# Kernel tuning notes

Measured on AMD Instinct MI355X. Metric: run time of the kernel, lower is better.

Reference implementation:

```python
import jax, jax.numpy as jnp
import numpy as np

T, K, H, I, E = 8192, 2, 1024, 2816, 8


def setup_inputs() -> dict:
    key = jax.random.key(0)
    k1, k2, k3, k4, k5 = jax.random.split(key, 5)
    hidden_states = jax.random.normal(k1, (T, H), dtype=jnp.float32)
    expert_routing_table = jax.random.randint(k2, (T, K), 0, E)
    router_weights = jax.random.uniform(k3, (T, K), dtype=jnp.float32)
    # permuted_weights=True: weights stored so forward is x @ w
    # w13: fused gate+up proj [E, H, 2I]; w2: down proj [E, I, H]
    w13 = jax.random.normal(k4, (E, H, 2 * I), dtype=jnp.float32) * (1.0 / np.sqrt(H))
    w2 = jax.random.normal(k5, (E, I, H), dtype=jnp.float32) * (1.0 / np.sqrt(I))
    return {
        "hidden_states": hidden_states,
        "expert_routing_table": expert_routing_table,
        "router_weights": router_weights,
        "w13": w13,
        "w2": w2,
    }


def reference(hidden_states, expert_routing_table, router_weights, w13, w2):
    # Semantics of hpu.mixture_of_experts with activation='silu':
    # out[t] = sum_k rw[t,k] * ( (silu(x@w1g[e]) * (x@w1u[e])) @ w2[e] ), e = table[t,k]
    n_experts = w13.shape[0]
    inter = w2.shape[1]
    # per-token combine coefficient for each expert: [T, E]
    onehot = jax.nn.one_hot(expert_routing_table, n_experts, dtype=hidden_states.dtype)  # [T,K,E]
    coeff = jnp.einsum("tke,tk->te", onehot, router_weights)
    out = jnp.zeros_like(hidden_states)
    for e in range(n_experts):
        gu = hidden_states @ w13[e]            # [T, 2I]
        gate, up = gu[:, :inter], gu[:, inter:]
        h = jax.nn.silu(gate) * up             # [T, I]
        out = out + coeff[:, e:e + 1] * (h @ w2[e])
    return out
```

## Files before the change

### kernel.cpp

```cpp
#include <hip/hip_runtime.h>

typedef unsigned short u16;
typedef unsigned int u32;
typedef __bf16 bf16x8 __attribute__((ext_vector_type(8)));
typedef float f32x4 __attribute__((ext_vector_type(4)));
typedef u16 u16x8 __attribute__((ext_vector_type(8)));

#define T_TOK 8192
#define HDIM 1024
#define IDIM 2816
#define NEXP 8
#define NPAIR (T_TOK * 2)
#define MAXRB 71

#define XB_OFF   (147456u)
#define W13T_OFF (XB_OFF + 16777216u)
#define W2T_OFF  (W13T_OFF + 92274688u)
#define H_OFF    (W2T_OFF + 46137344u)
#define WS_NEED  ((size_t)H_OFF + 102367232u)

__device__ __forceinline__ u16 f2bf(float f) {
  u32 u = __builtin_bit_cast(u32, f);
  u32 r = u + 0x7fffu + ((u >> 16) & 1u);
  return (u16)(r >> 16);
}

#define GLD16(g, l) __builtin_amdgcn_global_load_lds( \
    (const __attribute__((address_space(1))) void*)(g), \
    (__attribute__((address_space(3))) void*)(l), 16, 0, 0)

#define WAITVM(N) asm volatile("s_waitcnt vmcnt(" #N ")" ::: "memory")

__device__ __forceinline__ void sbar() {
  asm volatile("" ::: "memory");
  __builtin_amdgcn_s_barrier();
  asm volatile("" ::: "memory");
}

__device__ __forceinline__ void pbar() {
  __builtin_amdgcn_sched_barrier(0);
  asm volatile("" ::: "memory");
  __builtin_amdgcn_s_barrier();
  asm volatile("" ::: "memory");
  __builtin_amdgcn_sched_barrier(0);
}

__global__ void fillinit_k(int* __restrict__ pairs, int* __restrict__ meta) {
  if (blockIdx.x == 0 && threadIdx.x < 16) meta[threadIdx.x] = 0;
  pairs[blockIdx.x * 256 + threadIdx.x] = -1;
}

__global__ void count_k(const int* __restrict__ routing, int* __restrict__ meta) {
  int i = blockIdx.x * 256 + threadIdx.x;
  if (i < NPAIR) atomicAdd(&meta[routing[i]], 1);
}

__global__ void scan_k(int* __restrict__ meta) {
  if (threadIdx.x == 0) {
    int rb = 0;
    for (int e = 0; e < NEXP; ++e) {
      meta[16 + e] = rb * 256;
      int nrb = (meta[e] + 255) >> 8;
      for (int i = 0; i < nrb; ++i) meta[32 + rb + i] = e;
      rb += nrb;
    }
    meta[24] = rb;
  }
}

__global__ void scatter_k(const int* __restrict__ routing, int* __restrict__ meta,
                          int* __restrict__ pairs, int* __restrict__ inv) {
  int i = blockIdx.x * 256 + threadIdx.x;
  if (i < NPAIR) {
    int e = routing[i];
    int pos = atomicAdd(&meta[8 + e], 1);
    int row = meta[16 + e] + pos;
    pairs[row] = i;
    inv[i] = row;
  }
}

__global__ void conv_x(const float* __restrict__ in, u16* __restrict__ out) {
  int i = blockIdx.x * 256 + threadIdx.x;
  float4 a = ((const float4*)in)[2 * i];
  float4 b = ((const float4*)in)[2 * i + 1];
  u16x8 o = { f2bf(a.x), f2bf(a.y), f2bf(a.z), f2bf(a.w),
              f2bf(b.x), f2bf(b.y), f2bf(b.z), f2bf(b.w) };
  ((u16x8*)out)[i] = o;
}

#define TSW(r, c) (((((c) >> 2) ^ ((((r) >> 4) & 3) << 2)) << 2) | ((c) & 3))
__global__ void transpose_cvt(const float* __restrict__ in, u16* __restrict__ out,
                              int R, int C) {
  __shared__ float tile[64][68];
  size_t base = (size_t)blockIdx.z * (size_t)R * (size_t)C;
  in += base; out += base;
  int t = threadIdx.x;
  int r0 = blockIdx.y * 64, c0 = blockIdx.x * 64;
  int lr = t >> 4, cb = t & 15;
#pragma unroll
  for (int p = 0; p < 4; ++p) {
    int row = p * 16 + lr;
    float4 v = *(const float4*)&in[(size_t)(r0 + row) * C + c0 + cb * 4];
    int pc = ((cb ^ ((p & 3) << 2)) << 2);
    tile[row][pc] = v.x; tile[row][pc + 1] = v.y;
    tile[row][pc + 2] = v.z; tile[row][pc + 3] = v.w;
  }
  __syncthreads();
  int oc = t >> 2, g0 = (t & 3) * 2;
#pragma unroll
  for (int gg = 0; gg < 2; ++gg) {
    int g = g0 + gg;
    u16x8 o = { f2bf(tile[g * 8 + 0][TSW(g * 8 + 0, oc)]), f2bf(tile[g * 8 + 1][TSW(g * 8 + 1, oc)]),
                f2bf(tile[g * 8 + 2][TSW(g * 8 + 2, oc)]), f2bf(tile[g * 8 + 3][TSW(g * 8 + 3, oc)]),
                f2bf(tile[g * 8 + 4][TSW(g * 8 + 4, oc)]), f2bf(tile[g * 8 + 5][TSW(g * 8 + 5, oc)]),
                f2bf(tile[g * 8 + 6][TSW(g * 8 + 6, oc)]), f2bf(tile[g * 8 + 7][TSW(g * 8 + 7, oc)]) };
    *(u16x8*)&out[(size_t)(c0 + oc) * R + r0 + g * 8] = o;
  }
}

__global__ __launch_bounds__(512, 2) void gemm1_k(
    const u16* __restrict__ Xb, const u16* __restrict__ W13T,
    const int* __restrict__ pairs, const int* __restrict__ meta,
    const float* __restrict__ rwf, u16* __restrict__ Hb) {
  int lin = blockIdx.x + 22 * blockIdx.y;
  int xcd = lin & 7, slot = lin >> 3;
  int flat = (xcd < 2) ? xcd * 196 + slot : 392 + (xcd - 2) * 195 + slot;
  int bx = flat / 71, rb = flat % 71;
  if (rb >= meta[24]) return;
  const int e = meta[32 + rb];
  const int bn0 = bx * 128;
  const int tid = threadIdx.x, lane = tid & 63, w = tid >> 6;
  const int wr = w >> 2, wc = w & 3;
  const int rowBase = rb * 256;

  __shared__ __align__(16) u16 lds[65536];
  char* const lb = (char*)lds;

  const int tr = tid >> 3;
  const int swk = ((tid & 7) << 4) ^ ((tr & 7) << 4);
  const u16* aS[4]; const u16* bS[4];
  const u16* wBase = W13T + (size_t)e * (2 * IDIM) * HDIM;
#pragma unroll
  for (int s = 0; s < 4; ++s) {
    int pr = pairs[rowBase + s * 64 + tr];
    int tok = pr < 0 ? 0 : (pr >> 1);
    aS[s] = Xb + (size_t)tok * HDIM + (swk >> 1);
    bS[s] = wBase + (size_t)((tr >> 5) * IDIM + bn0 + s * 32 + (tr & 31)) * HDIM + (swk >> 1);
  }

#define STGA(b, h, kt) { GLD16(aS[(h)*2]   + (kt)*64, lb + (b)*32768 + (h)*16384 + tid*16); \
                         GLD16(aS[(h)*2+1] + (kt)*64, lb + (b)*32768 + (h)*16384 + 8192 + tid*16); }
#define STGB(b, h, kt) { GLD16(bS[(h)*2]   + (kt)*64, lb + 65536 + (b)*32768 + (h)*16384 + tid*16); \
                         GLD16(bS[(h)*2+1] + (kt)*64, lb + 65536 + (b)*32768 + (h)*16384 + 8192 + tid*16); }

  const int l15 = lane & 15, l4 = lane >> 4, l7 = lane & 7;
  const int ko0 = (l4 * 16) ^ (l7 << 4);
  const int ko1 = (64 + l4 * 16) ^ (l7 << 4);
  const int aFB = wr * 16384 + l15 * 128;
  const int bFB = 65536 + (wc * 64 + l15) * 128;

#define LDA(d, b, mh, mf, ko) d = *(const bf16x8*)(lb + (b)*32768 + aFB + (mh)*8192 + (mf)*2048 + (ko))
#define LDB(d, b, nf, ko)     d = *(const bf16x8*)(lb + (b)*32768 + bFB + (nf)*2048 + (ko))

#define MFQ(mh, A, B) \
  _Pragma("unroll") for (int mf = 0; mf < 4; ++mf) \
  _Pragma("unroll") for (int nf = 0; nf < 4; ++nf) \
    acc[(mh)*4+mf][nf] = __builtin_amdgcn_mfma_f32_16x16x32_bf16(A[mf], B[nf], acc[(mh)*4+mf][nf], 0, 0, 0);

  f32x4 acc[8][4];
  const f32x4 fz = {0.f, 0.f, 0.f, 0.f};
#pragma unroll
  for (int i = 0; i < 8; ++i)
#pragma unroll
    for (int j = 0; j < 4; ++j) acc[i][j] = fz;

  STGB(0, 0, 0); STGB(0, 1, 0); STGA(0, 0, 0); STGA(0, 1, 0); STGB(1, 0, 1); STGB(1, 1, 1);
  WAITVM(4);
  sbar();

  bf16x8 aA[4], aB[4], bK0[4], bK1[4];
#pragma unroll
  for (int f = 0; f < 4; ++f) { LDA(aA[f], 0, 0, f, ko0); LDB(bK0[f], 0, f, ko0); }

#define TILE1(b, t1, t2) { \
     \
    _Pragma("unroll") for (int f = 0; f < 4; ++f) { LDA(aB[f], b, 0, f, ko1); LDB(bK1[f], b, f, ko1); } \
    STGA((b)^1, 0, t1); \
    sbar(); \
    __builtin_amdgcn_s_setprio(1); MFQ(0, aA, bK0); __builtin_amdgcn_s_setprio(0); \
    sbar(); \
     \
    _Pragma("unroll") for (int f = 0; f < 4; ++f) { LDA(aA[f], b, 1, f, ko0); } \
    STGA((b)^1, 1, t1); \
    sbar(); \
    __builtin_amdgcn_s_setprio(1); MFQ(0, aB, bK1); __builtin_amdgcn_s_setprio(0); \
    sbar(); \
     \
    _Pragma("unroll") for (int f = 0; f < 4; ++f) { LDA(aB[f], b, 1, f, ko1); } \
    STGB(b, 0, t2); \
    sbar(); \
    __builtin_amdgcn_s_setprio(1); MFQ(1, aA, bK0); __builtin_amdgcn_s_setprio(0); \
    sbar(); \
     \
    WAITVM(2); \
    _Pragma("unroll") for (int f = 0; f < 4; ++f) { LDA(aA[f], (b)^1, 0, f, ko0); LDB(bK0[f], (b)^1, f, ko0); } \
    STGB(b, 1, t2); \
    sbar(); \
    __builtin_amdgcn_s_setprio(1); MFQ(1, aB, bK1); __builtin_amdgcn_s_setprio(0); \
    sbar(); \
  }

  for (int jj = 0; jj < 8; ++jj) {
    const int ta = (2 * jj + 1) & 15, tb = (2 * jj + 2) & 15, tc = (2 * jj + 3) & 15;
    TILE1(0, ta, tb);
    TILE1(1, tb, tc);
  }
#undef TILE1
#undef STGA
#undef STGB
#undef LDA
#undef LDB
#undef MFQ

  const int ct = l4;
#pragma unroll
  for (int mf = 0; mf < 8; ++mf) {
#pragma unroll
    for (int j = 0; j < 4; ++j) {
      int m = wr * 128 + mf * 16 + ct * 4 + j;
      int pr = rowBase + m;
      int pair = pairs[pr];
      float rw = pair >= 0 ? rwf[pair] : 0.f;
      u16* hrow = Hb + (size_t)pr * IDIM + bn0 + wc * 32 + l15;
#pragma unroll
      for (int g = 0; g < 2; ++g) {
        float gv = acc[mf][g][j], uv = acc[mf][g + 2][j];
        float s = gv / (1.f + __expf(-gv));
        hrow[g * 16] = f2bf(s * uv * rw);
      }
    }
  }
}

__global__ __launch_bounds__(256, 2) void gemm2_k(
    const u16* __restrict__ Hb, const u16* __restrict__ W2T,
    const int* __restrict__ meta, float* __restrict__ part) {
  int lin = blockIdx.y + 142 * blockIdx.x;
  int xcd = lin & 7, slot = lin >> 3;
  int flat = xcd * 142 + slot;
  int bx = flat / 142, rb2 = flat % 142;
  if (rb2 >= meta[24] * 2) return;
  const int e = meta[32 + (rb2 >> 1)];
  const int bn0 = bx * 128;
  const int tid = threadIdx.x, lane = tid & 63, w = tid >> 6;
  const int wr = w >> 1, wc = w & 1;
  const int rowBase = rb2 * 128;

  __shared__ __align__(16) u16 lds2[32768];
  char* const lb = (char*)lds2;

  const int sr = tid >> 3;
  const int swk = ((tid & 7) << 4) ^ ((sr & 7) << 4);
  const u16* aS[4]; const u16* bS[4];
#pragma unroll
  for (int j = 0; j < 4; ++j) {
    aS[j] = Hb + (size_t)(rowBase + j * 32 + sr) * IDIM + (swk >> 1);
    bS[j] = W2T + (size_t)e * HDIM * IDIM + (size_t)(bn0 + j * 32 + sr) * IDIM + (swk >> 1);
  }

#define STG_A2(b, kt) { GLD16(aS[0] + (kt)*64, lb + (b)*16384 + tid*16); \
                        GLD16(aS[1] + (kt)*64, lb + (b)*16384 + 4096 + tid*16); \
                        GLD16(aS[2] + (kt)*64, lb + (b)*16384 + 8192 + tid*16); \
                        GLD16(aS[3] + (kt)*64, lb + (b)*16384 + 12288 + tid*16); }
#define STG_B2(b, kt) { GLD16(bS[0] + (kt)*64, lb + 32768 + (b)*16384 + tid*16); \
                        GLD16(bS[1] + (kt)*64, lb + 32768 + (b)*16384 + 4096 + tid*16); \
                        GLD16(bS[2] + (kt)*64, lb + 32768 + (b)*16384 + 8192 + tid*16); \
                        GLD16(bS[3] + (kt)*64, lb + 32768 + (b)*16384 + 12288 + tid*16); }

  const int l15 = lane & 15, l4 = lane >> 4, l7 = lane & 7;
  const int ko0 = (l4 * 16) ^ (l7 << 4);
  const int ko1 = (64 + l4 * 16) ^ (l7 << 4);
  const int aFB = (wr * 64 + l15) * 128;
  const int bFB = (wc * 64 + l15) * 128;

#define LDAF2(d, b, mf, ko) d = *(const bf16x8*)(lb + (b)*16384 + aFB + (mf)*2048 + (ko))
#define LDBF2(d, b, nf, ko) d = *(const bf16x8*)(lb + 32768 + (b)*16384 + bFB + (nf)*2048 + (ko))

#define MF16v(A, B) \
  _Pragma("unroll") for (int mf = 0; mf < 4; ++mf) \
  _Pragma("unroll") for (int nf = 0; nf < 4; ++nf) \
    acc[mf][nf] = __builtin_amdgcn_mfma_f32_16x16x32_bf16(A[mf], B[nf], acc[mf][nf], 0, 0, 0);

  f32x4 acc[4][4];
  const f32x4 fz = {0.f, 0.f, 0.f, 0.f};
#pragma unroll
  for (int i = 0; i < 4; ++i)
#pragma unroll
    for (int j = 0; j < 4; ++j) acc[i][j] = fz;

  STG_A2(0, 0); STG_B2(0, 0); STG_A2(1, 1);
  WAITVM(4);
  pbar();

  bf16x8 a0[4], a1[4], b0[4], b1[4];
  for (int i = 0; i < 22; ++i) {
    const int t1 = 2 * i + 1;
    const int nt0 = (2 * i + 2 < 44) ? 2 * i + 2 : 0;
    const int nt1 = (2 * i + 3 < 44) ? 2 * i + 3 : 0;
#pragma unroll
    for (int f = 0; f < 4; ++f) { LDAF2(a0[f], 0, f, ko0); LDAF2(a1[f], 0, f, ko1);
                                  LDBF2(b0[f], 0, f, ko0); LDBF2(b1[f], 0, f, ko1); }
    STG_B2(1, t1);
    pbar();
    __builtin_amdgcn_s_setprio(1); MF16v(a0, b0); __builtin_amdgcn_s_setprio(0);
    pbar();
    STG_A2(0, nt0);
    pbar();
    __builtin_amdgcn_s_setprio(1); MF16v(a1, b1); __builtin_amdgcn_s_setprio(0);
    WAITVM(4);
    pbar();
#pragma unroll
    for (int f = 0; f < 4; ++f) { LDAF2(a0[f], 1, f, ko0); LDAF2(a1[f], 1, f, ko1);
                                  LDBF2(b0[f], 1, f, ko0); LDBF2(b1[f], 1, f, ko1); }
    STG_B2(0, nt0);
    pbar();
    __builtin_amdgcn_s_setprio(1); MF16v(a0, b0); __builtin_amdgcn_s_setprio(0);
    pbar();
    STG_A2(1, nt1);
    pbar();
    __builtin_amdgcn_s_setprio(1); MF16v(a1, b1); __builtin_amdgcn_s_setprio(0);
    WAITVM(4);
    pbar();
  }
#undef STG_A2
#undef STG_B2
#undef LDAF2
#undef LDBF2
#undef MF16v

  WAITVM(0);
  const int ct = l4;
#pragma unroll
  for (int mf = 0; mf < 4; ++mf) {
#pragma unroll
    for (int j = 0; j < 4; ++j) {
      int m = rowBase + wr * 64 + mf * 16 + ct * 4 + j;
      float* prow = part + (size_t)m * HDIM + bn0 + wc * 64 + l15;
#pragma unroll
      for (int nf = 0; nf < 4; ++nf) prow[nf * 16] = acc[mf][nf][j];
    }
  }
}

__global__ void reduce_k(const float* __restrict__ part, const int* __restrict__ inv,
                         float* __restrict__ out) {
  int t = blockIdx.x;
  int c = threadIdx.x * 4;
  int r0 = inv[2 * t], r1 = inv[2 * t + 1];
  float4 a = *(const float4*)&part[(size_t)r0 * HDIM + c];
  float4 b = *(const float4*)&part[(size_t)r1 * HDIM + c];
  float4 o = { a.x + b.x, a.y + b.y, a.z + b.z, a.w + b.w };
  *(float4*)&out[(size_t)t * HDIM + c] = o;
}

extern "C" void kernel_launch(void* const* d_in, const int* in_sizes, int n_in,
                              void* d_out, int out_size, void* d_ws, size_t ws_size,
                              hipStream_t stream) {
  const float* X = (const float*)d_in[0];
  const int* routing = (const int*)d_in[1];
  const float* rwf = (const float*)d_in[2];
  const float* w13 = (const float*)d_in[3];
  const float* w2 = (const float*)d_in[4];
  float* out = (float*)d_out;
  char* ws = (char*)d_ws;

  if (ws_size < WS_NEED) {
    hipMemsetAsync(d_out, 0, (size_t)T_TOK * HDIM * sizeof(float), stream);
    return;
  }

  int* meta = (int*)ws;
  int* pairs = (int*)(ws + 1024);
  int* inv = (int*)(ws + 73728);
  u16* Xb = (u16*)(ws + XB_OFF);
  u16* W13T = (u16*)(ws + W13T_OFF);
  u16* W2T = (u16*)(ws + W2T_OFF);
  u16* Hb = (u16*)(ws + H_OFF);
  float* part = (float*)(ws + W13T_OFF);

  fillinit_k<<<MAXRB, 256, 0, stream>>>(pairs, meta);
  count_k<<<NPAIR / 256, 256, 0, stream>>>(routing, meta);
  scan_k<<<1, 64, 0, stream>>>(meta);
  scatter_k<<<NPAIR / 256, 256, 0, stream>>>(routing, meta, pairs, inv);
  conv_x<<<(T_TOK * HDIM / 8) / 256, 256, 0, stream>>>(X, Xb);
  transpose_cvt<<<dim3(5632 / 64, 1024 / 64, NEXP), 256, 0, stream>>>(w13, W13T, 1024, 5632);
  transpose_cvt<<<dim3(1024 / 64, 2816 / 64, NEXP), 256, 0, stream>>>(w2, W2T, 2816, 1024);
  gemm1_k<<<dim3(22, MAXRB), 512, 0, stream>>>(Xb, W13T, pairs, meta, rwf, Hb);
  gemm2_k<<<dim3(8, 2 * MAXRB), 256, 0, stream>>>(Hb, W2T, meta, part);
  reduce_k<<<T_TOK, 256, 0, stream>>>(part, inv, out);
}
```

Before: 575.9 us.

## Restructure down-projection GEMM to 256x256 tiles with split-K and bf16 partials

The down-projection GEMM now runs 512-thread blocks with 256x256 output tiles, reusing the gemm1 pipelined schedule. The K dimension is split in two (1408 each) to keep the grid size up, and partial results are written as bf16 into two partial buffers. The reduce kernel sums four bf16 partials per output element. This targets better operand reuse per block and less partial-write traffic, at the cost of bf16 rounding of the partial sums and a larger LDS footprint, which may limit occupancy.

```diff
diff --git a/kernel.cpp b/kernel.cpp
--- a/kernel.cpp
+++ b/kernel.cpp
@@ -12,6 +12,8 @@
 #define NEXP 8
 #define NPAIR (T_TOK * 2)
 #define MAXRB 71
+#define PADROWS (MAXRB * 256)
+#define PARTSZ ((size_t)PADROWS * HDIM)
 
 #define XB_OFF   (147456u)
 #define W13T_OFF (XB_OFF + 16777216u)
@@ -24,6 +26,10 @@
   u32 r = u + 0x7fffu + ((u >> 16) & 1u);
   return (u16)(r >> 16);
 }
+__device__ __forceinline__ float bf2f(u16 v) {
+  u32 u = ((u32)v) << 16;
+  return __builtin_bit_cast(float, u);
+}
 
 #define GLD16(g, l) __builtin_amdgcn_global_load_lds( \
     (const __attribute__((address_space(1))) void*)(g), \
@@ -35,14 +41,6 @@
   asm volatile("" ::: "memory");
   __builtin_amdgcn_s_barrier();
   asm volatile("" ::: "memory");
-}
-
-__device__ __forceinline__ void pbar() {
-  __builtin_amdgcn_sched_barrier(0);
-  asm volatile("" ::: "memory");
-  __builtin_amdgcn_s_barrier();
-  asm volatile("" ::: "memory");
-  __builtin_amdgcn_sched_barrier(0);
 }
 
 __global__ void fillinit_k(int* __restrict__ pairs, int* __restrict__ meta) {
@@ -184,25 +182,21 @@
   for (int f = 0; f < 4; ++f) { LDA(aA[f], 0, 0, f, ko0); LDB(bK0[f], 0, f, ko0); }
 
 #define TILE1(b, t1, t2) { \
-     \
     _Pragma("unroll") for (int f = 0; f < 4; ++f) { LDA(aB[f], b, 0, f, ko1); LDB(bK1[f], b, f, ko1); } \
     STGA((b)^1, 0, t1); \
     sbar(); \
     __builtin_amdgcn_s_setprio(1); MFQ(0, aA, bK0); __builtin_amdgcn_s_setprio(0); \
     sbar(); \
-     \
     _Pragma("unroll") for (int f = 0; f < 4; ++f) { LDA(aA[f], b, 1, f, ko0); } \
     STGA((b)^1, 1, t1); \
     sbar(); \
     __builtin_amdgcn_s_setprio(1); MFQ(0, aB, bK1); __builtin_amdgcn_s_setprio(0); \
     sbar(); \
-     \
     _Pragma("unroll") for (int f = 0; f < 4; ++f) { LDA(aB[f], b, 1, f, ko1); } \
     STGB(b, 0, t2); \
     sbar(); \
     __builtin_amdgcn_s_setprio(1); MFQ(1, aA, bK0); __builtin_amdgcn_s_setprio(0); \
     sbar(); \
-     \
     WAITVM(2); \
     _Pragma("unroll") for (int f = 0; f < 4; ++f) { LDA(aA[f], (b)^1, 0, f, ko0); LDB(bK0[f], (b)^1, f, ko0); } \
     STGB(b, 1, t2); \
@@ -217,11 +211,6 @@
     TILE1(1, tb, tc);
   }
 #undef TILE1
-#undef STGA
-#undef STGB
-#undef LDA
-#undef LDB
-#undef MFQ
 
   const int ct = l4;
 #pragma unroll
@@ -241,127 +230,148 @@
       }
     }
   }
-}
-
-__global__ __launch_bounds__(256, 2) void gemm2_k(
+#undef STGA
+#undef STGB
+#undef LDA
+#undef LDB
+#undef MFQ
+}
+
+__global__ __launch_bounds__(512, 2) void gemm2_k(
     const u16* __restrict__ Hb, const u16* __restrict__ W2T,
-    const int* __restrict__ meta, float* __restrict__ part) {
-  int lin = blockIdx.y + 142 * blockIdx.x;
+    const int* __restrict__ meta, u16* __restrict__ part) {
+  int lin = blockIdx.x + 4 * blockIdx.y + 284 * blockIdx.z;
   int xcd = lin & 7, slot = lin >> 3;
-  int flat = xcd * 142 + slot;
-  int bx = flat / 142, rb2 = flat % 142;
-  if (rb2 >= meta[24] * 2) return;
-  const int e = meta[32 + (rb2 >> 1)];
-  const int bn0 = bx * 128;
+  int flat = xcd * 71 + slot;
+  int kz = flat / 284, rm = flat % 284;
+  int bx = rm / 71, rb = rm % 71;
+  if (rb >= meta[24]) return;
+  const int e = meta[32 + rb];
+  const int bn0 = bx * 256;
+  const int kz0 = kz * 1408;
   const int tid = threadIdx.x, lane = tid & 63, w = tid >> 6;
-  const int wr = w >> 1, wc = w & 1;
-  const int rowBase = rb2 * 128;
-
-  __shared__ __align__(16) u16 lds2[32768];
-  char* const lb = (char*)lds2;
-
-  const int sr = tid >> 3;
-  const int swk = ((tid & 7) << 4) ^ ((sr & 7) << 4);
+  const int wr = w >> 2, wc = w & 3;
+  const int rowBase = rb * 256;
+
+  __shared__ __align__(16) u16 lds[65536];
+  char* const lb = (char*)lds;
+
+  const int tr = tid >> 3;
+  const int swk = ((tid & 7) << 4) ^ ((tr & 7) << 4);
   const u16* aS[4]; const u16* bS[4];
-#pragma unroll
-  for (int j = 0; j < 4; ++j) {
-    aS[j] = Hb + (size_t)(rowBase + j * 32 + sr) * IDIM + (swk >> 1);
-    bS[j] = W2T + (size_t)e * HDIM * IDIM + (size_t)(bn0 + j * 32 + sr) * IDIM + (swk >> 1);
-  }
-
-#define STG_A2(b, kt) { GLD16(aS[0] + (kt)*64, lb + (b)*16384 + tid*16); \
-                        GLD16(aS[1] + (kt)*64, lb + (b)*16384 + 4096 + tid*16); \
-                        GLD16(aS[2] + (kt)*64, lb + (b)*16384 + 8192 + tid*16); \
-                        GLD16(aS[3] + (kt)*64, lb + (b)*16384 + 12288 + tid*16); }
-#define STG_B2(b, kt) { GLD16(bS[0] + (kt)*64, lb + 32768 + (b)*16384 + tid*16); \
-                        GLD16(bS[1] + (kt)*64, lb + 32768 + (b)*16384 + 4096 + tid*16); \
-                        GLD16(bS[2] + (kt)*64, lb + 32768 + (b)*16384 + 8192 + tid*16); \
-                        GLD16(bS[3] + (kt)*64, lb + 32768 + (b)*16384 + 12288 + tid*16); }
+  const u16* w2Base = W2T + (size_t)e * HDIM * IDIM;
+#pragma unroll
+  for (int s = 0; s < 4; ++s) {
+    aS[s] = Hb + (size_t)(rowBase + s * 64 + tr) * IDIM + kz0 + (swk >> 1);
+    bS[s] = w2Base + (size_t)(bn0 + s * 64 + tr) * IDIM + kz0 + (swk >> 1);
+  }
+
+#define STGA(b, h, kt) { GLD16(aS[(h)*2]   + (kt)*64, lb + (b)*32768 + (h)*16384 + tid*16); \
+                         GLD16(aS[(h)*2+1] + (kt)*64, lb + (b)*32768 + (h)*16384 + 8192 + tid*16); }
+#define STGB(b, h, kt) { GLD16(bS[(h)*2]   + (kt)*64, lb + 65536 + (b)*32768 + (h)*16384 + tid*16); \
+                         GLD16(bS[(h)*2+1] + (kt)*64, lb + 65536 + (b)*32768 + (h)*16384 + 8192 + tid*16); }
 
   const int l15 = lane & 15, l4 = lane >> 4, l7 = lane & 7;
   const int ko0 = (l4 * 16) ^ (l7 << 4);
   const int ko1 = (64 + l4 * 16) ^ (l7 << 4);
-  const int aFB = (wr * 64 + l15) * 128;
-  const int bFB = (wc * 64 + l15) * 128;
-
-#define LDAF2(d, b, mf, ko) d = *(const bf16x8*)(lb + (b)*16384 + aFB + (mf)*2048 + (ko))
-#define LDBF2(d, b, nf, ko) d = *(const bf16x8*)(lb + 32768 + (b)*16384 + bFB + (nf)*2048 + (ko))
-
-#define MF16v(A, B) \
+  const int aFB = wr * 16384 + l15 * 128;
+  const int bFB = 65536 + (wc * 64 + l15) * 128;
+
+#define LDA(d, b, mh, mf, ko) d = *(const bf16x8*)(lb + (b)*32768 + aFB + (mh)*8192 + (mf)*2048 + (ko))
+#define LDB(d, b, nf, ko)     d = *(const bf16x8*)(lb + (b)*32768 + bFB + (nf)*2048 + (ko))
+
+#define MFQ(mh, A, B) \
   _Pragma("unroll") for (int mf = 0; mf < 4; ++mf) \
   _Pragma("unroll") for (int nf = 0; nf < 4; ++nf) \
-    acc[mf][nf] = __builtin_amdgcn_mfma_f32_16x16x32_bf16(A[mf], B[nf], acc[mf][nf], 0, 0, 0);
-
-  f32x4 acc[4][4];
+    acc[(mh)*4+mf][nf] = __builtin_amdgcn_mfma_f32_16x16x32_bf16(A[mf], B[nf], acc[(mh)*4+mf][nf], 0, 0, 0);
+
+  f32x4 acc[8][4];
   const f32x4 fz = {0.f, 0.f, 0.f, 0.f};
 #pragma unroll
-  for (int i = 0; i < 4; ++i)
+  for (int i = 0; i < 8; ++i)
 #pragma unroll
     for (int j = 0; j < 4; ++j) acc[i][j] = fz;
 
-  STG_A2(0, 0); STG_B2(0, 0); STG_A2(1, 1);
+  STGB(0, 0, 0); STGB(0, 1, 0); STGA(0, 0, 0); STGA(0, 1, 0); STGB(1, 0, 1); STGB(1, 1, 1);
   WAITVM(4);
-  pbar();
-
-  bf16x8 a0[4], a1[4], b0[4], b1[4];
-  for (int i = 0; i < 22; ++i) {
-    const int t1 = 2 * i + 1;
-    const int nt0 = (2 * i + 2 < 44) ? 2 * i + 2 : 0;
-    const int nt1 = (2 * i + 3 < 44) ? 2 * i + 3 : 0;
-#pragma unroll
-    for (int f = 0; f < 4; ++f) { LDAF2(a0[f], 0, f, ko0); LDAF2(a1[f], 0, f, ko1);
-                                  LDBF2(b0[f], 0, f, ko0); LDBF2(b1[f], 0, f, ko1); }
-    STG_B2(1, t1);
-    pbar();
-    __builtin_amdgcn_s_setprio(1); MF16v(a0, b0); __builtin_amdgcn_s_setprio(0);
-    pbar();
-    STG_A2(0, nt0);
-    pbar();
-    __builtin_amdgcn_s_setprio(1); MF16v(a1, b1); __builtin_amdgcn_s_setprio(0);
-    WAITVM(4);
-    pbar();
-#pragma unroll
-    for (int f = 0; f < 4; ++f) { LDAF2(a0[f], 1, f, ko0); LDAF2(a1[f], 1, f, ko1);
-                                  LDBF2(b0[f], 1, f, ko0); LDBF2(b1[f], 1, f, ko1); }
-    STG_B2(0, nt0);
-    pbar();
-    __builtin_amdgcn_s_setprio(1); MF16v(a0, b0); __builtin_amdgcn_s_setprio(0);
-    pbar();
-    STG_A2(1, nt1);
-    pbar();
-    __builtin_amdgcn_s_setprio(1); MF16v(a1, b1); __builtin_amdgcn_s_setprio(0);
-    WAITVM(4);
-    pbar();
-  }
-#undef STG_A2
-#undef STG_B2
-#undef LDAF2
-#undef LDBF2
-#undef MF16v
-
-  WAITVM(0);
+  sbar();
+
+  bf16x8 aA[4], aB[4], bK0[4], bK1[4];
+#pragma unroll
+  for (int f = 0; f < 4; ++f) { LDA(aA[f], 0, 0, f, ko0); LDB(bK0[f], 0, f, ko0); }
+
+#define TILE2(b, t1, t2) { \
+    _Pragma("unroll") for (int f = 0; f < 4; ++f) { LDA(aB[f], b, 0, f, ko1); LDB(bK1[f], b, f, ko1); } \
+    STGA((b)^1, 0, t1); \
+    sbar(); \
+    __builtin_amdgcn_s_setprio(1); MFQ(0, aA, bK0); __builtin_amdgcn_s_setprio(0); \
+    sbar(); \
+    _Pragma("unroll") for (int f = 0; f < 4; ++f) { LDA(aA[f], b, 1, f, ko0); } \
+    STGA((b)^1, 1, t1); \
+    sbar(); \
+    __builtin_amdgcn_s_setprio(1); MFQ(0, aB, bK1); __builtin_amdgcn_s_setprio(0); \
+    sbar(); \
+    _Pragma("unroll") for (int f = 0; f < 4; ++f) { LDA(aB[f], b, 1, f, ko1); } \
+    STGB(b, 0, t2); \
+    sbar(); \
+    __builtin_amdgcn_s_setprio(1); MFQ(1, aA, bK0); __builtin_amdgcn_s_setprio(0); \
+    sbar(); \
+    WAITVM(2); \
+    _Pragma("unroll") for (int f = 0; f < 4; ++f) { LDA(aA[f], (b)^1, 0, f, ko0); LDB(bK0[f], (b)^1, f, ko0); } \
+    STGB(b, 1, t2); \
+    sbar(); \
+    __builtin_amdgcn_s_setprio(1); MFQ(1, aB, bK1); __builtin_amdgcn_s_setprio(0); \
+    sbar(); \
+  }
+
+  for (int jj = 0; jj < 11; ++jj) {
+    int ta = 2 * jj + 1; if (ta >= 22) ta -= 22;
+    int tb = 2 * jj + 2; if (tb >= 22) tb -= 22;
+    int tc = 2 * jj + 3; if (tc >= 22) tc -= 22;
+    TILE2(0, ta, tb);
+    TILE2(1, tb, tc);
+  }
+#undef TILE2
+#undef STGA
+#undef STGB
+#undef LDA
+#undef LDB
+#undef MFQ
+
   const int ct = l4;
-#pragma unroll
-  for (int mf = 0; mf < 4; ++mf) {
+  u16* pz = part + (size_t)kz * PARTSZ;
+#pragma unroll
+  for (int mf = 0; mf < 8; ++mf) {
 #pragma unroll
     for (int j = 0; j < 4; ++j) {
-      int m = rowBase + wr * 64 + mf * 16 + ct * 4 + j;
-      float* prow = part + (size_t)m * HDIM + bn0 + wc * 64 + l15;
-#pragma unroll
-      for (int nf = 0; nf < 4; ++nf) prow[nf * 16] = acc[mf][nf][j];
+      int m = wr * 128 + mf * 16 + ct * 4 + j;
+      u16* prow = pz + (size_t)(rowBase + m) * HDIM + bn0 + wc * 64 + l15;
+#pragma unroll
+      for (int nf = 0; nf < 4; ++nf) prow[nf * 16] = f2bf(acc[mf][nf][j]);
     }
   }
 }
 
-__global__ void reduce_k(const float* __restrict__ part, const int* __restrict__ inv,
+__global__ void reduce_k(const u16* __restrict__ part, const int* __restrict__ inv,
                          float* __restrict__ out) {
   int t = blockIdx.x;
-  int c = threadIdx.x * 4;
+  int c = threadIdx.x * 8;
   int r0 = inv[2 * t], r1 = inv[2 * t + 1];
-  float4 a = *(const float4*)&part[(size_t)r0 * HDIM + c];
-  float4 b = *(const float4*)&part[(size_t)r1 * HDIM + c];
-  float4 o = { a.x + b.x, a.y + b.y, a.z + b.z, a.w + b.w };
-  *(float4*)&out[(size_t)t * HDIM + c] = o;
+  u16x8 a0 = *(const u16x8*)&part[(size_t)r0 * HDIM + c];
+  u16x8 a1 = *(const u16x8*)&part[(size_t)r1 * HDIM + c];
+  u16x8 b0 = *(const u16x8*)&part[PARTSZ + (size_t)r0 * HDIM + c];
+  u16x8 b1 = *(const u16x8*)&part[PARTSZ + (size_t)r1 * HDIM + c];
+  float4 o0, o1;
+  o0.x = bf2f(a0[0]) + bf2f(a1[0]) + bf2f(b0[0]) + bf2f(b1[0]);
+  o0.y = bf2f(a0[1]) + bf2f(a1[1]) + bf2f(b0[1]) + bf2f(b1[1]);
+  o0.z = bf2f(a0[2]) + bf2f(a1[2]) + bf2f(b0[2]) + bf2f(b1[2]);
+  o0.w = bf2f(a0[3]) + bf2f(a1[3]) + bf2f(b0[3]) + bf2f(b1[3]);
+  o1.x = bf2f(a0[4]) + bf2f(a1[4]) + bf2f(b0[4]) + bf2f(b1[4]);
+  o1.y = bf2f(a0[5]) + bf2f(a1[5]) + bf2f(b0[5]) + bf2f(b1[5]);
+  o1.z = bf2f(a0[6]) + bf2f(a1[6]) + bf2f(b0[6]) + bf2f(b1[6]);
+  o1.w = bf2f(a0[7]) + bf2f(a1[7]) + bf2f(b0[7]) + bf2f(b1[7]);
+  *(float4*)&out[(size_t)t * HDIM + c] = o0;
+  *(float4*)&out[(size_t)t * HDIM + c + 4] = o1;
 }
 
 extern "C" void kernel_launch(void* const* d_in, const int* in_sizes, int n_in,
@@ -387,7 +397,7 @@
   u16* W13T = (u16*)(ws + W13T_OFF);
   u16* W2T = (u16*)(ws + W2T_OFF);
   u16* Hb = (u16*)(ws + H_OFF);
-  float* part = (float*)(ws + W13T_OFF);
+  u16* part = (u16*)(ws + W13T_OFF);
 
   fillinit_k<<<MAXRB, 256, 0, stream>>>(pairs, meta);
   count_k<<<NPAIR / 256, 256, 0, stream>>>(routing, meta);
@@ -397,6 +407,6 @@
   transpose_cvt<<<dim3(5632 / 64, 1024 / 64, NEXP), 256, 0, stream>>>(w13, W13T, 1024, 5632);
   transpose_cvt<<<dim3(1024 / 64, 2816 / 64, NEXP), 256, 0, stream>>>(w2, W2T, 2816, 1024);
   gemm1_k<<<dim3(22, MAXRB), 512, 0, stream>>>(Xb, W13T, pairs, meta, rwf, Hb);
-  gemm2_k<<<dim3(8, 2 * MAXRB), 256, 0, stream>>>(Hb, W2T, meta, part);
-  reduce_k<<<T_TOK, 256, 0, stream>>>(part, inv, out);
-}
+  gemm2_k<<<dim3(4, MAXRB, 2), 512, 0, stream>>>(Hb, W2T, meta, part);
+  reduce_k<<<T_TOK, 128, 0, stream>>>(part, inv, out);
+}
```

Result: no change. 581.0 us (+0.9%).
